# Optimization experiments

Hardware: AMD Instinct MI355X
Metric: run time of the kernel (lower is better)

The kernel has to match this reference:

```python
import jax, jax.numpy as jnp
import numpy as np

EPS = 1e-5
K_NBR = 21   # num_neighbors + 1 (self)
PSI = 4


def _bn(x, g, b):
    # BatchNorm (training-mode forward): channel-last, normalize over all other axes
    axes = tuple(range(x.ndim - 1))
    m = jnp.mean(x, axis=axes, keepdims=True)
    v = jnp.var(x, axis=axes, keepdims=True)
    return (x - m) * jax.lax.rsqrt(v + EPS) * g + b


def setup_inputs() -> dict:
    key = jax.random.key(0)
    ks = jax.random.split(key, 16)
    B, N, Cin, Cout = 4, 2048, 64, 256
    h = Cout // 2
    w_ch = Cout // PSI
    heads = 2 * PSI - 1

    def w(k, o, i):
        return jax.random.normal(k, (o, i), dtype=jnp.float32) * (1.0 / np.sqrt(i))

    p = {}
    p['xyz'] = jax.random.normal(ks[0], (B, N, 3), dtype=jnp.float32)
    p['f'] = jax.random.normal(ks[1], (B, Cin, N), dtype=jnp.float32)
    p['W_geo'] = w(ks[2], h, 6);       p['g_geo'] = jnp.ones(h);   p['b_geo'] = jnp.zeros(h)
    p['W_feat'] = w(ks[3], h, 2 * Cin); p['g_feat'] = jnp.ones(h); p['b_feat'] = jnp.zeros(h)
    p['g_bn'] = jnp.ones(Cout); p['b_bn'] = jnp.zeros(Cout)
    p['W_q'] = w(ks[4], Cout, Cout); p['g_q'] = jnp.ones(Cout); p['b_q'] = jnp.zeros(Cout)
    p['W_k'] = w(ks[5], Cout, Cout); p['g_k'] = jnp.ones(Cout); p['b_k'] = jnp.zeros(Cout)
    p['W_v'] = w(ks[6], Cout, Cout); p['g_v'] = jnp.ones(Cout); p['b_v'] = jnp.zeros(Cout)
    p['W_fus'] = w(ks[7], Cout, heads * w_ch); p['bias_fus'] = jnp.zeros(Cout)
    p['g_fus'] = jnp.ones(Cout); p['b_fus'] = jnp.zeros(Cout)
    p['g_ln'] = jnp.ones(Cout); p['b_ln'] = jnp.zeros(Cout)
    p['W_mlp'] = w(ks[8], Cout, Cout); p['bias_mlp'] = jnp.zeros(Cout)
    return p


def reference(xyz, f, W_geo, g_geo, b_geo, W_feat, g_feat, b_feat, g_bn, b_bn,
              W_q, g_q, b_q, W_k, g_k, b_k, W_v, g_v, b_v,
              W_fus, bias_fus, g_fus, b_fus, g_ln, b_ln, W_mlp, bias_mlp):
    B, N, _ = xyz.shape
    Cout = g_bn.shape[0]
    w_ch = Cout // PSI
    d_sh = w_ch // 2
    heads = 2 * PSI - 1

    # ---- PositionFusion: KNN grouping ----
    sq = jnp.sum(xyz * xyz, axis=-1)                                   # [B,N]
    d2 = sq[:, :, None] + sq[:, None, :] - 2.0 * jnp.einsum('bnd,bmd->bnm', xyz, xyz)
    _, idx = jax.lax.top_k(-d2, K_NBR)                                 # [B,N,K]

    grouped_xyz = jax.vmap(lambda p, i: p[i])(xyz, idx)                # [B,N,K,3]
    xyz_diff = grouped_xyz - xyz[:, :, None, :]
    geo_in = jnp.concatenate(
        [jnp.broadcast_to(xyz[:, :, None, :], grouped_xyz.shape), xyz_diff], axis=-1)  # [B,N,K,6]

    ft = jnp.transpose(f, (0, 2, 1))                                   # [B,N,Cin]
    grouped_f = jax.vmap(lambda p, i: p[i])(ft, idx)                   # [B,N,K,Cin]
    feat_in = jnp.concatenate(
        [grouped_f, jnp.broadcast_to(ft[:, :, None, :], grouped_f.shape)], axis=-1)    # [B,N,K,2Cin]

    geo = jax.nn.relu(_bn(jnp.einsum('bnki,oi->bnko', geo_in, W_geo), g_geo, b_geo))
    fea = jax.nn.relu(_bn(jnp.einsum('bnki,oi->bnko', feat_in, W_feat), g_feat, b_feat))
    feature_ = jnp.max(jnp.concatenate([geo, fea], axis=-1), axis=2)   # [B,N,Cout] (maxpool over K)

    # ---- BatchNorm1d ----
    x = _bn(feature_, g_bn, b_bn)

    # ---- Shifted-channel multi-head attention ----
    q = jax.nn.relu(_bn(jnp.einsum('bnc,oc->bno', x, W_q), g_q, b_q))
    k = jax.nn.relu(_bn(jnp.einsum('bnc,oc->bno', x, W_k), g_k, b_k))
    v = jax.nn.relu(_bn(jnp.einsum('bnc,oc->bno', x, W_v), g_v, b_v))

    qh = jnp.stack([q[..., m * d_sh:m * d_sh + w_ch] for m in range(heads)], axis=1)  # [B,H,N,w]
    kh = jnp.stack([k[..., m * d_sh:m * d_sh + w_ch] for m in range(heads)], axis=1)
    vh = jnp.stack([v[..., m * d_sh:m * d_sh + w_ch] for m in range(heads)], axis=1)

    a = jax.nn.softmax(jnp.einsum('bhnc,bhmc->bhnm', qh, kh), axis=-1)  # [B,H,N,N]
    o = jnp.einsum('bhnm,bhmc->bhnc', a, vh)                            # [B,H,N,w]
    O = jnp.transpose(o, (0, 2, 1, 3)).reshape(B, N, heads * w_ch)      # channel-concat per head

    fus = jax.nn.relu(_bn(jnp.einsum('bnc,oc->bno', O, W_fus) + bias_fus, g_fus, b_fus))

    feature__ = fus + feature_                                          # residual

    # ---- LayerNorm over channels ----
    m = jnp.mean(feature__, axis=-1, keepdims=True)
    var = jnp.var(feature__, axis=-1, keepdims=True)
    y = (feature__ - m) * jax.lax.rsqrt(var + EPS) * g_ln + b_ln

    out = feature__ + (jnp.einsum('bnc,oc->bno', y, W_mlp) + bias_mlp)
    return jnp.transpose(out, (0, 2, 1))                                # [B,Cout,N] like torch
```

## Files before the change

kernel.cpp:

```cpp
#include <hip/hip_runtime.h>
#include <math.h>

#define NB    4
#define NPTS  2048
#define ROWS  (NB*NPTS)
#define CIN   64
#define COUT  256
#define KNBR  21
#define NHEADS 7
#define WCH   64
#define DSH   32
#define LOG2E 1.4426950408889634f

typedef __attribute__((ext_vector_type(8))) short short8;
typedef __attribute__((ext_vector_type(4))) float floatx4;

#if __has_builtin(__builtin_amdgcn_exp2f)
#define EXP2(x) __builtin_amdgcn_exp2f(x)
#else
#define EXP2(x) __expf((x)*0.6931471805599453f)
#endif
#if __has_builtin(__builtin_amdgcn_rcpf)
#define RCP(x) __builtin_amdgcn_rcpf(x)
#else
#define RCP(x) (1.0f/(x))
#endif

__device__ __forceinline__ ushort f2bf(float x) {
    unsigned u = __float_as_uint(x);
    u += 0x7fffu + ((u >> 16) & 1u);
    return (ushort)(u >> 16);
}

__device__ __forceinline__ unsigned cvt_pk_bf16(float lo, float hi) {
    unsigned r;
    asm("v_cvt_pk_bf16_f32 %0, %1, %2" : "=v"(r) : "v"(lo), "v"(hi));
    return r;
}

template<int CTRL, int RMASK>
__device__ __forceinline__ unsigned dpp_umin_step(unsigned x) {
    unsigned t = (unsigned)__builtin_amdgcn_update_dpp((int)x, (int)x, CTRL, RMASK, 0xF, false);
    return (t < x) ? t : x;
}
__device__ __forceinline__ unsigned wave_min_u32(unsigned x) {
    x = dpp_umin_step<0x111, 0xF>(x);
    x = dpp_umin_step<0x112, 0xF>(x);
    x = dpp_umin_step<0x114, 0xF>(x);
    x = dpp_umin_step<0x118, 0xF>(x);
    x = dpp_umin_step<0x142, 0xA>(x);
    x = dpp_umin_step<0x143, 0xC>(x);
    return (unsigned)__builtin_amdgcn_readlane((int)x, 63);
}

__device__ __forceinline__ unsigned umin2(unsigned a, unsigned b) { return a < b ? a : b; }
__device__ __forceinline__ unsigned umax2(unsigned a, unsigned b) { return a < b ? b : a; }

__device__ __forceinline__ void ins6(unsigned &m1, unsigned &m2, unsigned &m3,
                                     unsigned &m4, unsigned &m5, unsigned &m6, unsigned k) {
    unsigned c = k, t;
    t = umin2(m1, c); c = umax2(m1, c); m1 = t;
    t = umin2(m2, c); c = umax2(m2, c); m2 = t;
    t = umin2(m3, c); c = umax2(m3, c); m3 = t;
    t = umin2(m4, c); c = umax2(m4, c); m4 = t;
    t = umin2(m5, c); c = umax2(m5, c); m5 = t;
    m6 = umin2(m6, c);
}

__global__ __launch_bounds__(256) void prep_knn(const float* __restrict__ f, const float* __restrict__ Wf,
                                                const float* __restrict__ xyz, const float* __restrict__ Wg,
                                                const float* __restrict__ W_q, const float* __restrict__ W_k,
                                                const float* __restrict__ W_v, const float* __restrict__ W_fus,
                                                float* __restrict__ X, float* __restrict__ A,
                                                ushort* __restrict__ Wb, float* __restrict__ sums,
                                                int* __restrict__ idx) {
    __shared__ float4 SXQ[2048];
    int t = threadIdx.x;
    int blk = blockIdx.x;
    if (blk < 512) {
        float* As = (float*)SXQ;
        float* Ws = As + 16*68;
        int bx = blk & 127, by = blk >> 7;
        if (by == 0 && bx < 12) sums[bx*256 + t] = 0.f;
        int gid = (by*128 + bx)*256 + t;
        for (int i = gid; i < 311296; i += 131072) {
            const float* Wsrc; int off;
            if (i < 65536)       { Wsrc = W_q;   off = i; }
            else if (i < 131072) { Wsrc = W_k;   off = i - 65536; }
            else if (i < 196608) { Wsrc = W_v;   off = i - 131072; }
            else                 { Wsrc = W_fus; off = i - 196608; }
            Wb[i] = f2bf(Wsrc[off]);
        }
        int r0 = bx * 64, n0 = by * 64;
        for (int e = t; e < 4096; e += 256) {
            int row = r0 + (e >> 6), c = n0 + (e & 63), cc = c & 127;
            float x = xyz[row*3], y = xyz[row*3+1], z = xyz[row*3+2];
            const float* w = Wg + cc*6;
            float s = (c < 128) ? ((w[3]*x + w[4]*y) + w[5]*z)
                                : (((w[0]-w[3])*x + (w[1]-w[4])*y) + (w[2]-w[5])*z);
            A[(size_t)row*256 + c] = s;
        }
        int b = r0 >> 11, nbase = r0 & 2047;
        int tx = t & 15, ty = t >> 4;
        float acc[4][4];
#pragma unroll
        for (int i = 0; i < 4; i++)
#pragma unroll
            for (int j = 0; j < 4; j++) acc[i][j] = 0.f;
        int m64 = t & 63, kg = t >> 6;
        int lk = t & 15, lm = t >> 4;
        for (int k0 = 0; k0 < 64; k0 += 16) {
#pragma unroll
            for (int p = 0; p < 4; p++) {
                int k = kg*4 + p;
                As[k*68 + m64] = f[(size_t)b*CIN*NPTS + (size_t)(k0 + k)*NPTS + nbase + m64];
            }
#pragma unroll
            for (int i2 = 0; i2 < 4; i2++) {
                int cg = n0 + lm + 16*i2;
                Ws[lk*68 + lm + 16*i2] = Wf[(size_t)(cg & 127)*128 + (cg >> 7)*64 + k0 + lk];
            }
            __syncthreads();
#pragma unroll
            for (int kq = 0; kq < 16; kq++) {
                float4 a  = *(const float4*)&As[kq*68 + 4*ty];
                float4 b4 = *(const float4*)&Ws[kq*68 + 4*tx];
                float av[4] = {a.x, a.y, a.z, a.w};
                float bv[4] = {b4.x, b4.y, b4.z, b4.w};
#pragma unroll
                for (int i = 0; i < 4; i++)
#pragma unroll
                    for (int j = 0; j < 4; j++) acc[i][j] = fmaf(av[i], bv[j], acc[i][j]);
            }
            __syncthreads();
        }
#pragma unroll
        for (int i = 0; i < 4; i++)
#pragma unroll
            for (int j = 0; j < 4; j++)
                X[(size_t)(r0 + 4*ty + i)*256 + n0 + 4*tx + j] = acc[i][j];
        return;
    }
    int kb = blk - 512;
    int b = kb >> 9;
    int g = kb & 511;
    for (int m = t; m < NPTS; m += 256) {
        float x = xyz[(size_t)b*NPTS*3 + m*3];
        float y = xyz[(size_t)b*NPTS*3 + m*3 + 1];
        float z = xyz[(size_t)b*NPTS*3 + m*3 + 2];
        SXQ[m] = make_float4(x, y, z, (x*x + y*y) + z*z);
    }
    __syncthreads();
    int w = t >> 6, lane = t & 63;
    int n = g*4 + w;
    float4 q4 = SXQ[n];
    float qx = q4.x, qy = q4.y, qz = q4.z, sqn = q4.w;

    unsigned key[32];
    unsigned a1 = 0xFFFFFFFFu, a2 = 0xFFFFFFFFu, a3 = 0xFFFFFFFFu,
             a4 = 0xFFFFFFFFu, a5 = 0xFFFFFFFFu, a6 = 0xFFFFFFFFu;
    unsigned c1 = 0xFFFFFFFFu, c2 = 0xFFFFFFFFu, c3 = 0xFFFFFFFFu,
             c4 = 0xFFFFFFFFu, c5 = 0xFFFFFFFFu, c6 = 0xFFFFFFFFu;
#pragma unroll
    for (int i = 0; i < 16; i++) {
        int m = lane + (i << 6);
        float4 p = SXQ[m];
        float dt = (qx*p.x + qy*p.y) + qz*p.z;
        float d2 = fmaxf((sqn + p.w) - 2.0f*dt, 0.f);
        unsigned kv = (__float_as_uint(d2) & 0xFFFFF800u) | (unsigned)m;
        key[i] = kv;
        ins6(a1, a2, a3, a4, a5, a6, kv);
    }
#pragma unroll
    for (int i = 16; i < 32; i++) {
        int m = lane + (i << 6);
        float4 p = SXQ[m];
        float dt = (qx*p.x + qy*p.y) + qz*p.z;
        float d2 = fmaxf((sqn + p.w) - 2.0f*dt, 0.f);
        unsigned kv = (__float_as_uint(d2) & 0xFFFFF800u) | (unsigned)m;
        key[i] = kv;
        ins6(c1, c2, c3, c4, c5, c6, kv);
    }
    ins6(a1, a2, a3, a4, a5, a6, c1);
    ins6(a1, a2, a3, a4, a5, a6, c2);
    ins6(a1, a2, a3, a4, a5, a6, c3);
    ins6(a1, a2, a3, a4, a5, a6, c4);
    ins6(a1, a2, a3, a4, a5, a6, c5);
    ins6(a1, a2, a3, a4, a5, a6, c6);

    unsigned winkey = 0xFFFFFFFFu;
    {
        unsigned fr = a1, p2 = a2, p3 = a3, p4 = a4, p5 = a5, p6 = a6;
#pragma unroll
        for (int kk = 0; kk < 32; kk++) {
            unsigned win = wave_min_u32(fr);
            if (lane == kk) winkey = win;
            bool own = (fr == win);
            fr = own ? p2 : fr;
            p2 = own ? p3 : p2;
            p3 = own ? p4 : p3;
            p4 = own ? p5 : p4;
            p5 = own ? p6 : p5;
            p6 = own ? 0xFFFFFFFFu : p6;
        }
        if (__ballot(fr == 0xFFFFFFFFu) != 0ULL) {
            winkey = 0xFFFFFFFFu;
            for (int kk = 0; kk < 32; kk++) {
                unsigned lv = key[0];
#pragma unroll
                for (int i = 1; i < 32; i++) lv = (key[i] < lv) ? key[i] : lv;
                unsigned win = wave_min_u32(lv);
                if (lane == kk) winkey = win;
                unsigned widx = win & 2047u;
                int slot = (int)(widx >> 6);
                bool own = (lane == (int)(widx & 63u));
#pragma unroll
                for (int i = 0; i < 32; i++)
                    if (i == slot && own) key[i] = 0xFFFFFFFFu;
            }
        }
    }
    double d2r;
    int mr;
    {
        double qx64 = (double)qx, qy64 = (double)qy, qz64 = (double)qz;
        double sqn64 = qx64*qx64 + qy64*qy64 + qz64*qz64;
        if (lane < 32) {
            mr = (int)(winkey & 2047u);
            float4 p = SXQ[mr];
            double x = (double)p.x, y = (double)p.y, z = (double)p.z;
            double sqm = x*x + y*y + z*z;
            double dt  = qx64*x + qy64*y + qz64*z;
            d2r = (sqn64 + sqm) - 2.0*dt;
        } else {
            d2r = INFINITY; mr = 0x7FFFFFFF;
        }
    }
#pragma unroll
    for (int k = 2; k <= 32; k <<= 1) {
#pragma unroll
        for (int j = k >> 1; j > 0; j >>= 1) {
            double od = __shfl_xor(d2r, j, 64);
            int    om = __shfl_xor(mr, j, 64);
            bool up    = ((lane & k) == 0);
            bool lower = ((lane & j) == 0);
            bool oless = (od < d2r) || (od == d2r && om < mr);
            bool keepOther = up ? (lower ? oless : !oless) : (lower ? !oless : oless);
            if (keepOther) { d2r = od; mr = om; }
        }
    }
    if (lane < KNBR)
        idx[((size_t)b*NPTS + n)*KNBR + lane] = mr;
}

__global__ __launch_bounds__(256) void stats_gf(const float* __restrict__ geoBC, const float* __restrict__ featAC,
                                                const int* __restrict__ idx, const float* __restrict__ g_geo,
                                                const float* __restrict__ g_feat,
                                                float* __restrict__ sums, float* __restrict__ xsel) {
    int c = threadIdx.x;
    int cc = c & 127;
    const float* base = (c < 128) ? geoBC : featAC;
    bool wantmax = ((c < 128) ? g_geo[cc] : g_feat[cc]) >= 0.f;
    float s = 0.f, ss = 0.f;
    int r0 = blockIdx.x * 32;
    for (int r = r0; r < r0 + 32; r++) {
        int b = r >> 11;
        float ctr = base[(size_t)r*256 + 128 + cc];
        float mx = -1e30f, mn = 1e30f;
        const int* ip = idx + (size_t)r*KNBR;
        for (int kk = 0; kk < KNBR; kk++) {
            int j = ip[kk];
            float xv = ctr + base[((size_t)(b*NPTS + j))*256 + cc];
            mx = fmaxf(mx, xv); mn = fminf(mn, xv);
            s += xv; ss += xv*xv;
        }
        xsel[(size_t)r*256 + c] = wantmax ? mx : mn;
    }
    atomicAdd(&sums[c], s);
    atomicAdd(&sums[256 + c], ss);
}

__global__ __launch_bounds__(256) void feature_maxsel(const float* __restrict__ xsel, const float* __restrict__ sums,
                                                      const float* __restrict__ g_geo, const float* __restrict__ b_geo,
                                                      const float* __restrict__ g_feat, const float* __restrict__ b_feat,
                                                      float* __restrict__ feat, float* __restrict__ sums_bn1) {
    int c = threadIdx.x;
    const float inv = 1.0f / (float)(ROWS*KNBR);
    float mean = sums[c]*inv;
    float var  = sums[256+c]*inv - mean*mean;
    float g  = (c < 128) ? g_geo[c] : g_feat[c-128];
    float bb = (c < 128) ? b_geo[c] : b_feat[c-128];
    float sc = g / sqrtf(var + 1e-5f);
    float tt = bb - mean*sc;
    float s = 0.f, ss = 0.f;
    int r0 = blockIdx.x*32;
    for (int r = r0; r < r0+32; r++) {
        size_t i = (size_t)r*256 + c;
        float y = fmaxf(fmaf(sc, xsel[i], tt), 0.f);
        feat[i] = y; s += y; ss += y*y;
    }
    atomicAdd(&sums_bn1[c], s); atomicAdd(&sums_bn1[256+c], ss);
}

__global__ __launch_bounds__(256) void gemm_qkv(const float* __restrict__ Af, const float* __restrict__ sums_in,
                                                const float* __restrict__ g_bn, const float* __restrict__ b_bn,
                                                const ushort* __restrict__ Wb,
                                                float* __restrict__ QKVF, float* __restrict__ sums) {
    __shared__ float bns[2][256];
    __shared__ float red[4][256][2];
    int t = threadIdx.x;
    int r0 = blockIdx.x * 64, g = blockIdx.y;
    int w = t >> 6, lane = t & 63;
    int r15 = lane & 15, quad = lane >> 4;
    {
        float mean = sums_in[512 + t] * (1.0f/(float)ROWS);
        float var  = sums_in[768 + t] * (1.0f/(float)ROWS) - mean*mean;
        float sc = g_bn[t] / sqrtf(var + 1e-5f);
        bns[0][t] = sc;
        bns[1][t] = b_bn[t] - mean*sc;
    }
    __syncthreads();
    short8 aq[8];
    {
        const float* ap = Af + (size_t)(r0 + 16*w + r15)*256;
#pragma unroll
        for (int kc = 0; kc < 8; kc++) {
            int k0 = 32*kc + 8*quad;
            float4 a0 = *(const float4*)&ap[k0];
            float4 a1 = *(const float4*)&ap[k0+4];
            float4 s0 = *(const float4*)&bns[0][k0];
            float4 s1 = *(const float4*)&bns[0][k0+4];
            float4 h0 = *(const float4*)&bns[1][k0];
            float4 h1 = *(const float4*)&bns[1][k0+4];
            ushort u8[8];
            u8[0] = f2bf(fmaf(s0.x, a0.x, h0.x)); u8[1] = f2bf(fmaf(s0.y, a0.y, h0.y));
            u8[2] = f2bf(fmaf(s0.z, a0.z, h0.z)); u8[3] = f2bf(fmaf(s0.w, a0.w, h0.w));
            u8[4] = f2bf(fmaf(s1.x, a1.x, h1.x)); u8[5] = f2bf(fmaf(s1.y, a1.y, h1.y));
            u8[6] = f2bf(fmaf(s1.z, a1.z, h1.z)); u8[7] = f2bf(fmaf(s1.w, a1.w, h1.w));
            aq[kc] = *(short8*)u8;
        }
    }
    floatx4 zero4 = {0.f, 0.f, 0.f, 0.f};
    floatx4 acc[16];
#pragma unroll
    for (int st = 0; st < 16; st++) acc[st] = zero4;
    const ushort* wbase = Wb + (size_t)g*65536 + (size_t)r15*256 + 8*quad;
#pragma unroll
    for (int st = 0; st < 16; st++) {
        const ushort* wp = wbase + (size_t)(16*st)*256;
#pragma unroll
        for (int kc = 0; kc < 8; kc++) {
            short8 bf = *(const short8*)(wp + 32*kc);
            acc[st] = __builtin_amdgcn_mfma_f32_16x16x32_bf16(aq[kc], bf, acc[st], 0, 0, 0);
        }
    }
#pragma unroll
    for (int st = 0; st < 16; st++) {
        float s  = (acc[st][0] + acc[st][1]) + (acc[st][2] + acc[st][3]);
        float q2 = (acc[st][0]*acc[st][0] + acc[st][1]*acc[st][1]) +
                   (acc[st][2]*acc[st][2] + acc[st][3]*acc[st][3]);
        s  += __shfl_xor(s, 16, 64);  s  += __shfl_xor(s, 32, 64);
        q2 += __shfl_xor(q2, 16, 64); q2 += __shfl_xor(q2, 32, 64);
        if (lane < 16) { red[w][16*st + r15][0] = s; red[w][16*st + r15][1] = q2; }
#pragma unroll
        for (int reg = 0; reg < 4; reg++)
            QKVF[(size_t)(r0 + 16*w + 4*quad + reg)*768 + g*256 + 16*st + r15] = acc[st][reg];
    }
    __syncthreads();
    {
        float s = red[0][t][0] + red[1][t][0] + red[2][t][0] + red[3][t][0];
        float q = red[0][t][1] + red[1][t][1] + red[2][t][1] + red[3][t][1];
        atomicAdd(&sums[1024 + g*512 + t], s);
        atomicAdd(&sums[1024 + g*512 + 256 + t], q);
    }
}

__global__ __launch_bounds__(256) void affine_qkv(const float* __restrict__ QKVF, const float* __restrict__ sums,
                                                  const float* __restrict__ g_q, const float* __restrict__ b_q,
                                                  const float* __restrict__ g_k, const float* __restrict__ b_k,
                                                  const float* __restrict__ g_v, const float* __restrict__ b_v,
                                                  ushort* __restrict__ qk, ushort* __restrict__ vt) {
    __shared__ float sts[6][256];
    __shared__ ushort tile[64][72];
    int t = threadIdx.x;
    {
        const float* gs[3] = {g_q, g_k, g_v};
        const float* bs[3] = {b_q, b_k, b_v};
#pragma unroll
        for (int g = 0; g < 3; g++) {
            float mean = sums[1024 + g*512 + t] * (1.0f/(float)ROWS);
            float var  = sums[1024 + g*512 + 256 + t] * (1.0f/(float)ROWS) - mean*mean;
            float sc = gs[g][t] / sqrtf(var + 1e-5f);
            float sh = bs[g][t] - mean*sc;
            if (g == 0) { sc *= LOG2E; sh *= LOG2E; }
            sts[2*g][t] = sc;
            sts[2*g+1][t] = sh;
        }
    }
    __syncthreads();
    int r0 = blockIdx.x * 64, c0 = blockIdx.y * 64;
    int b = r0 >> 11, nbase = r0 & 2047;
    if (c0 < 512) {
#pragma unroll
        for (int rep = 0; rep < 16; rep++) {
            int e = t + 256*rep;
            int row = e >> 6, c = e & 63;
            int col = c0 + c, g = col >> 8, cc = col & 255;
            float v = QKVF[(size_t)(r0 + row)*768 + col];
            v = fmaxf(fmaf(sts[2*g][cc], v, sts[2*g+1][cc]), 0.f);
            qk[(size_t)(r0 + row)*512 + col] = f2bf(v);
        }
    } else {
#pragma unroll
        for (int rep = 0; rep < 16; rep++) {
            int e = t + 256*rep;
            int row = e >> 6, c = e & 63;
            int col = c0 + c, cc = col & 255;
            float v = QKVF[(size_t)(r0 + row)*768 + col];
            v = fmaxf(fmaf(sts[4][cc], v, sts[5][cc]), 0.f);
            tile[c][row] = f2bf(v);
        }
        __syncthreads();
#pragma unroll
        for (int rep = 0; rep < 16; rep++) {
            int e = t + 256*rep;
            int cc = e >> 6, nn = e & 63;
            vt[((size_t)(b*256 + (c0 - 512) + cc))*2048 + nbase + nn] = tile[cc][nn];
        }
    }
}

__global__ __launch_bounds__(256) void attn2(const ushort* __restrict__ qk, const ushort* __restrict__ vt,
                                             float* __restrict__ obuf) {
    __shared__ ushort Ksh[2][64*72];
    __shared__ ushort Psh[128*72];
    int h = blockIdx.y, b = blockIdx.z;
    int r0 = blockIdx.x * 128;
    int t = threadIdx.x;
    int w = t >> 6, lane = t & 63;
    int r15 = lane & 15, quad = lane >> 4;
    size_t rowbase = (size_t)b*NPTS;
    int hoff = h*DSH;

    int rr0 = t >> 3, c8 = t & 7;
    const ushort* ksrc = qk + (rowbase + rr0)*512 + 256 + hoff + 8*c8;
    int ldst = rr0*72 + 8*c8;

    const ushort* vsrc = vt + ((size_t)(b*256 + hoff + r15))*2048 + 8*quad;

    short8 aq[2][2];
#pragma unroll
    for (int u = 0; u < 2; u++)
#pragma unroll
        for (int s = 0; s < 2; s++)
            aq[u][s] = *(const short8*)(qk + (rowbase + r0 + 32*w + 16*u + r15)*512 + hoff + 32*s + 8*quad);

    {
        uint4 k0 = *(const uint4*)(ksrc);
        uint4 k1 = *(const uint4*)(ksrc + 32*512);
        *(uint4*)&Ksh[0][ldst] = k0;
        *(uint4*)&Ksh[0][ldst + 32*72] = k1;
    }

    floatx4 zero4 = {0.f, 0.f, 0.f, 0.f};
    floatx4 oacc[2][4];
    float mrun[2], lrun[2];
#pragma unroll
    for (int u = 0; u < 2; u++) {
        mrun[u] = -1e30f; lrun[u] = 0.f;
#pragma unroll
        for (int i = 0; i < 4; i++) oacc[u][i] = zero4;
    }

    ushort* prow0 = &Psh[(32*w + r15)*72];
    ushort* prow1 = &Psh[(32*w + 16 + r15)*72];

    asm volatile("s_waitcnt lgkmcnt(0)" ::: "memory");
    __builtin_amdgcn_s_barrier();
    __builtin_amdgcn_sched_barrier(0);

    int cur = 0;
    for (int m0 = 0; m0 < NPTS; m0 += 64) {
        int mnext = (m0 + 64 < NPTS) ? (m0 + 64) : 0;
        uint4 kreg0 = *(const uint4*)(ksrc + (size_t)mnext*512);
        uint4 kreg1 = *(const uint4*)(ksrc + (size_t)mnext*512 + 32*512);

        short8 vreg[2][4];
#pragma unroll
        for (int s = 0; s < 2; s++)
#pragma unroll
            for (int td = 0; td < 4; td++)
                vreg[s][td] = *(const short8*)(vsrc + (size_t)(16*td)*2048 + m0 + 32*s);

        const ushort* Kc = Ksh[cur];

        floatx4 sacc[2][4];
#pragma unroll
        for (int u = 0; u < 2; u++)
#pragma unroll
            for (int tt = 0; tt < 4; tt++) sacc[u][tt] = zero4;
        __builtin_amdgcn_s_setprio(1);
#pragma unroll
        for (int tt = 0; tt < 4; tt++) {
            int key = 16*tt + r15;
#pragma unroll
            for (int s = 0; s < 2; s++) {
                short8 kf = *(const short8*)&Kc[key*72 + 32*s + 8*quad];
                sacc[0][tt] = __builtin_amdgcn_mfma_f32_16x16x32_bf16(kf, aq[0][s], sacc[0][tt], 0, 0, 0);
                sacc[1][tt] = __builtin_amdgcn_mfma_f32_16x16x32_bf16(kf, aq[1][s], sacc[1][tt], 0, 0, 0);
            }
        }
        __builtin_amdgcn_s_setprio(0);

#pragma unroll
        for (int u = 0; u < 2; u++) {
            float mx = sacc[u][0][0];
#pragma unroll
            for (int tt = 0; tt < 4; tt++)
#pragma unroll
                for (int reg = 0; reg < 4; reg++) mx = fmaxf(mx, sacc[u][tt][reg]);
            mx = fmaxf(mx, __shfl_xor(mx, 16, 64));
            mx = fmaxf(mx, __shfl_xor(mx, 32, 64));

            if (!__all(mx <= mrun[u])) {
                float mnew = fmaxf(mrun[u], mx);
                float alpha = EXP2(mrun[u] - mnew);
                lrun[u] *= alpha;
#pragma unroll
                for (int td = 0; td < 4; td++) oacc[u][td] *= alpha;
                mrun[u] = mnew;
            }

            ushort* prow = u ? prow1 : prow0;
            float rs = 0.f;
#pragma unroll
            for (int tt = 0; tt < 4; tt++) {
                float p0 = EXP2(sacc[u][tt][0] - mrun[u]);
                float p1 = EXP2(sacc[u][tt][1] - mrun[u]);
                float p2 = EXP2(sacc[u][tt][2] - mrun[u]);
                float p3 = EXP2(sacc[u][tt][3] - mrun[u]);
                rs += (p0 + p1) + (p2 + p3);
                uint2 pk2;
                pk2.x = cvt_pk_bf16(p0, p1);
                pk2.y = cvt_pk_bf16(p2, p3);
                *(uint2*)&prow[16*tt + 4*quad] = pk2;
            }
            rs += __shfl_xor(rs, 16, 64);
            rs += __shfl_xor(rs, 32, 64);
            lrun[u] += rs;
        }

        __builtin_amdgcn_s_setprio(1);
#pragma unroll
        for (int s = 0; s < 2; s++) {
            short8 pf0 = *(const short8*)&prow0[32*s + 8*quad];
            short8 pf1 = *(const short8*)&prow1[32*s + 8*quad];
#pragma unroll
            for (int td = 0; td < 4; td++) {
                short8 vf = vreg[s][td];
                oacc[0][td] = __builtin_amdgcn_mfma_f32_16x16x32_bf16(vf, pf0, oacc[0][td], 0, 0, 0);
                oacc[1][td] = __builtin_amdgcn_mfma_f32_16x16x32_bf16(vf, pf1, oacc[1][td], 0, 0, 0);
            }
        }
        __builtin_amdgcn_s_setprio(0);

        *(uint4*)&Ksh[cur ^ 1][ldst] = kreg0;
        *(uint4*)&Ksh[cur ^ 1][ldst + 32*72] = kreg1;
        cur ^= 1;

        asm volatile("s_waitcnt lgkmcnt(0)" ::: "memory");
        __builtin_amdgcn_s_barrier();
        __builtin_amdgcn_sched_barrier(0);
    }

#pragma unroll
    for (int u = 0; u < 2; u++) {
        float invl = RCP(lrun[u]);
#pragma unroll
        for (int td = 0; td < 4; td++) {
            floatx4 o = oacc[u][td] * invl;
            *(float4*)&obuf[(rowbase + r0 + 32*w + 16*u + r15)*(size_t)(NHEADS*WCH) + h*WCH + 16*td + 4*quad] =
                *(float4*)&o;
        }
    }
}

__global__ __launch_bounds__(256) void gemm_fus(const float* __restrict__ OBUF, const ushort* __restrict__ Wb,
                                                const float* __restrict__ bias, float* __restrict__ C,
                                                float* __restrict__ sums) {
    __shared__ float red[4][128][2];
    int t = threadIdx.x;
    int r0 = blockIdx.x * 64, n0 = blockIdx.y * 128;
    int w = t >> 6, lane = t & 63;
    int r15 = lane & 15, quad = lane >> 4;
    int arow = 16*w + r15;
    short8 aq[14];
    {
        const float* p0 = OBUF + (size_t)(r0 + arow)*448;
#pragma unroll
        for (int kc = 0; kc < 14; kc++) {
            int k0 = 32*kc + 8*quad;
            float4 x0 = *(const float4*)&p0[k0];
            float4 y0 = *(const float4*)&p0[k0+4];
            ushort u8[8];
            u8[0] = f2bf(x0.x); u8[1] = f2bf(x0.y);
            u8[2] = f2bf(x0.z); u8[3] = f2bf(x0.w);
            u8[4] = f2bf(y0.x); u8[5] = f2bf(y0.y);
            u8[6] = f2bf(y0.z); u8[7] = f2bf(y0.w);
            aq[kc] = *(short8*)u8;
        }
    }
    floatx4 zero4 = {0.f, 0.f, 0.f, 0.f};
    floatx4 acc[8];
#pragma unroll
    for (int st = 0; st < 8; st++) acc[st] = zero4;
    const ushort* wbase = Wb + 196608 + (size_t)(n0 + r15)*448 + 8*quad;
#pragma unroll
    for (int st = 0; st < 8; st++) {
        const ushort* wp = wbase + (size_t)(16*st)*448;
#pragma unroll
        for (int kc = 0; kc < 14; kc++) {
            short8 bf = *(const short8*)(wp + 32*kc);
            acc[st] = __builtin_amdgcn_mfma_f32_16x16x32_bf16(aq[kc], bf, acc[st], 0, 0, 0);
        }
    }
#pragma unroll
    for (int st = 0; st < 8; st++) {
        int col = n0 + 16*st + r15;
        float bi = bias[col];
        float v0 = acc[st][0] + bi, v1 = acc[st][1] + bi, v2 = acc[st][2] + bi, v3 = acc[st][3] + bi;
        float s  = (v0 + v1) + (v2 + v3);
        float q2 = (v0*v0 + v1*v1) + (v2*v2 + v3*v3);
        s  += __shfl_xor(s, 16, 64);  s  += __shfl_xor(s, 32, 64);
        q2 += __shfl_xor(q2, 16, 64); q2 += __shfl_xor(q2, 32, 64);
        if (lane < 16) { red[w][16*st + r15][0] = s; red[w][16*st + r15][1] = q2; }
        C[(size_t)(r0 + 16*w + 4*quad + 0)*256 + col] = v0;
        C[(size_t)(r0 + 16*w + 4*quad + 1)*256 + col] = v1;
        C[(size_t)(r0 + 16*w + 4*quad + 2)*256 + col] = v2;
        C[(size_t)(r0 + 16*w + 4*quad + 3)*256 + col] = v3;
    }
    __syncthreads();
    {
        int col = t >> 1, which = t & 1;
        float v = red[0][col][which] + red[1][col][which] + red[2][col][which] + red[3][col][which];
        atomicAdd(&sums[2560 + which*256 + n0 + col], v);
    }
}

__global__ __launch_bounds__(256) void gemm_mlp_ln(const float* __restrict__ FUSP, const float* __restrict__ A,
                                                   const float* __restrict__ sums,
                                                   const float* __restrict__ g_fus, const float* __restrict__ b_fus,
                                                   const float* __restrict__ g_ln, const float* __restrict__ b_ln,
                                                   const float* __restrict__ W, const float* __restrict__ bias,
                                                   float* __restrict__ outp) {
    __shared__ float Ys[256][68];
    __shared__ float FFs[64][65];
    __shared__ float Ws[16][68];
    __shared__ float tr[64][65];
    __shared__ float SC[256], SH[256], GL[256], BL[256];
    int t = threadIdx.x;
    int r0 = blockIdx.x*64, n0 = blockIdx.y*64;
    {
        float mean0 = sums[2560 + t] * (1.0f/(float)ROWS);
        float var0  = sums[2560 + 256 + t] * (1.0f/(float)ROWS) - mean0*mean0;
        float sc = g_fus[t] / sqrtf(var0 + 1e-5f);
        SC[t] = sc; SH[t] = b_fus[t] - mean0*sc;
        GL[t] = g_ln[t]; BL[t] = b_ln[t];
    }
    __syncthreads();
    int row = t >> 2, seg = t & 3;
    size_t rb = (size_t)(r0 + row)*256;
    float4 vv[16];
    float s = 0.f, ss = 0.f;
#pragma unroll
    for (int j = 0; j < 16; j++) {
        int c = seg*64 + 4*j;
        float4 fp = *(const float4*)&FUSP[rb + c];
        float4 fe = *(const float4*)&A[rb + c];
        float4 sc4 = *(const float4*)&SC[c];
        float4 sh4 = *(const float4*)&SH[c];
        float4 v;
        v.x = fmaxf(fmaf(sc4.x, fp.x, sh4.x), 0.f) + fe.x;
        v.y = fmaxf(fmaf(sc4.y, fp.y, sh4.y), 0.f) + fe.y;
        v.z = fmaxf(fmaf(sc4.z, fp.z, sh4.z), 0.f) + fe.z;
        v.w = fmaxf(fmaf(sc4.w, fp.w, sh4.w), 0.f) + fe.w;
        vv[j] = v;
        s  += (v.x + v.y) + (v.z + v.w);
        ss += (v.x*v.x + v.y*v.y) + (v.z*v.z + v.w*v.w);
        if (seg == blockIdx.y) *(float4*)&FFs[row][4*j] = v;
    }
    s  += __shfl_xor(s, 1, 64);  s  += __shfl_xor(s, 2, 64);
    ss += __shfl_xor(ss, 1, 64); ss += __shfl_xor(ss, 2, 64);
    float mean = s * (1.f/256.f);
    float var  = ss * (1.f/256.f) - mean*mean;
    float rin  = 1.f/sqrtf(var + 1e-5f);
#pragma unroll
    for (int j = 0; j < 16; j++) {
        int c = seg*64 + 4*j;
        float4 gl = *(const float4*)&GL[c];
        float4 bl = *(const float4*)&BL[c];
        float4 v = vv[j];
        Ys[c+0][row] = (v.x - mean)*rin*gl.x + bl.x;
        Ys[c+1][row] = (v.y - mean)*rin*gl.y + bl.y;
        Ys[c+2][row] = (v.z - mean)*rin*gl.z + bl.z;
        Ys[c+3][row] = (v.w - mean)*rin*gl.w + bl.w;
    }
    __syncthreads();
    int tx = t & 15, ty = t >> 4;
    int lk = t & 15, lm = t >> 4;
    float acc[4][4];
#pragma unroll
    for (int i = 0; i < 4; i++)
#pragma unroll
        for (int j = 0; j < 4; j++) acc[i][j] = 0.f;
    for (int k0 = 0; k0 < 256; k0 += 16) {
#pragma unroll
        for (int i2 = 0; i2 < 4; i2++)
            Ws[lk][lm + 16*i2] = W[(size_t)(n0 + lm + 16*i2)*256 + k0 + lk];
        __syncthreads();
#pragma unroll
        for (int kq = 0; kq < 16; kq++) {
            float4 a  = *(const float4*)&Ys[k0 + kq][4*ty];
            float4 b4 = *(const float4*)&Ws[kq][4*tx];
            float av[4] = {a.x, a.y, a.z, a.w};
            float bv[4] = {b4.x, b4.y, b4.z, b4.w};
#pragma unroll
            for (int i = 0; i < 4; i++)
#pragma unroll
                for (int j = 0; j < 4; j++) acc[i][j] = fmaf(av[i], bv[j], acc[i][j]);
        }
        __syncthreads();
    }
#pragma unroll
    for (int i = 0; i < 4; i++)
#pragma unroll
        for (int j = 0; j < 4; j++) {
            float v = acc[i][j] + bias[n0 + 4*tx + j] + FFs[4*ty + i][4*tx + j];
            tr[4*tx + j][4*ty + i] = v;
        }
    __syncthreads();
    int b = r0 >> 11, nbase = r0 & 2047;
#pragma unroll
    for (int rep = 0; rep < 16; rep++) {
        int e = t + 256*rep;
        int cl = e >> 6, nl = e & 63;
        outp[((size_t)(b*256 + n0 + cl))*2048 + nbase + nl] = tr[cl][nl];
    }
}

extern "C" void kernel_launch(void* const* d_in, const int* in_sizes, int n_in,
                              void* d_out, int out_size, void* d_ws, size_t ws_size,
                              hipStream_t stream) {
    const float* xyz    = (const float*)d_in[0];
    const float* f      = (const float*)d_in[1];
    const float* W_geo  = (const float*)d_in[2];
    const float* g_geo  = (const float*)d_in[3];
    const float* b_geo  = (const float*)d_in[4];
    const float* W_feat = (const float*)d_in[5];
    const float* g_feat = (const float*)d_in[6];
    const float* b_feat = (const float*)d_in[7];
    const float* g_bn   = (const float*)d_in[8];
    const float* b_bn   = (const float*)d_in[9];
    const float* W_q    = (const float*)d_in[10];
    const float* g_q    = (const float*)d_in[11];
    const float* b_q    = (const float*)d_in[12];
    const float* W_k    = (const float*)d_in[13];
    const float* g_k    = (const float*)d_in[14];
    const float* b_k    = (const float*)d_in[15];
    const float* W_v    = (const float*)d_in[16];
    const float* g_v    = (const float*)d_in[17];
    const float* b_v    = (const float*)d_in[18];
    const float* W_fus  = (const float*)d_in[19];
    const float* bias_fus = (const float*)d_in[20];
    const float* g_fus  = (const float*)d_in[21];
    const float* b_fus  = (const float*)d_in[22];
    const float* g_ln   = (const float*)d_in[23];
    const float* b_ln   = (const float*)d_in[24];
    const float* W_mlp  = (const float*)d_in[25];
    const float* bias_mlp = (const float*)d_in[26];

    float* ws = (float*)d_ws;
    const size_t MBF = 262144;
    float* SUMS  = ws;
    int*   IDX   = (int*)(ws + 16384);
    float* A     = ws + 1*MBF;
    float* X     = ws + 9*MBF;
    ushort* QK16 = (ushort*)(ws + 9*MBF);
    float* FUSP  = ws + 9*MBF;
    float* CSEL  = ws + 17*MBF;
    float* QKVF  = ws + 17*MBF;
    float* OBUF  = ws + 17*MBF;
    ushort* VT16 = (ushort*)(ws + 45*MBF);
    ushort* WB16 = (ushort*)(ws + 49*MBF);

    prep_knn<<<2560, 256, 0, stream>>>(f, W_feat, xyz, W_geo, W_q, W_k, W_v, W_fus,
                                       X, A, WB16, SUMS, IDX);
    stats_gf<<<256, 256, 0, stream>>>(A, X, IDX, g_geo, g_feat, SUMS, CSEL);
    feature_maxsel<<<256, 256, 0, stream>>>(CSEL, SUMS, g_geo, b_geo, g_feat, b_feat, A, SUMS + 512);
    gemm_qkv<<<dim3(128, 3), 256, 0, stream>>>(A, SUMS, g_bn, b_bn, WB16, QKVF, SUMS);
    affine_qkv<<<dim3(128, 12), 256, 0, stream>>>(QKVF, SUMS, g_q, b_q, g_k, b_k, g_v, b_v, QK16, VT16);
    attn2<<<dim3(NPTS/128, NHEADS, NB), 256, 0, stream>>>(QK16, VT16, OBUF);
    gemm_fus<<<dim3(128, 2), 256, 0, stream>>>(OBUF, WB16, bias_fus, FUSP, SUMS);
    gemm_mlp_ln<<<dim3(128, 4), 256, 0, stream>>>(FUSP, A, SUMS, g_fus, b_fus, g_ln, b_ln,
                                                  W_mlp, bias_mlp, (float*)d_out);
}
```

Baseline: 392.6 us.

## Stage V tiles in LDS and double query rows per attention block

The attention kernel now processes 256 query rows per block with 512 threads instead of 128 rows with 256 threads, halving the number of blocks per head. V tiles are cooperatively loaded into a double-buffered LDS array alongside K, rather than each wave loading its own V fragments straight from global memory. This is meant to cut redundant global K/V traffic and per-wave global load latency across the eight waves that share each tile. In exchange it uses more LDS per block, adds LDS reads for the V fragments, and reduces grid size to 224 blocks, which may underfill the GPU.

```diff
diff --git a/kernel.cpp b/kernel.cpp
--- a/kernel.cpp
+++ b/kernel.cpp
@@ -430,23 +430,23 @@
     }
 }
 
-__global__ __launch_bounds__(256) void attn2(const ushort* __restrict__ qk, const ushort* __restrict__ vt,
+__global__ __launch_bounds__(512) void attn2(const ushort* __restrict__ qk, const ushort* __restrict__ vt,
                                              float* __restrict__ obuf) {
     __shared__ ushort Ksh[2][64*72];
-    __shared__ ushort Psh[128*72];
+    __shared__ ushort Vts[2][64*72];
+    __shared__ ushort Psh[256*72];
     int h = blockIdx.y, b = blockIdx.z;
-    int r0 = blockIdx.x * 128;
+    int r0 = blockIdx.x * 256;
     int t = threadIdx.x;
     int w = t >> 6, lane = t & 63;
     int r15 = lane & 15, quad = lane >> 4;
     size_t rowbase = (size_t)b*NPTS;
     int hoff = h*DSH;
-
-    int rr0 = t >> 3, c8 = t & 7;
-    const ushort* ksrc = qk + (rowbase + rr0)*512 + 256 + hoff + 8*c8;
-    int ldst = rr0*72 + 8*c8;
-
-    const ushort* vsrc = vt + ((size_t)(b*256 + hoff + r15))*2048 + 8*quad;
+    int rr = t >> 3, c8 = t & 7;
+
+    const ushort* ksrc = qk + (rowbase + rr)*512 + 256 + hoff + 8*c8;
+    const ushort* vsrc = vt + ((size_t)(b*256 + hoff + rr))*2048 + 8*c8;
+    int ldst = rr*72 + 8*c8;
 
     short8 aq[2][2];
 #pragma unroll
@@ -457,9 +457,9 @@
 
     {
         uint4 k0 = *(const uint4*)(ksrc);
-        uint4 k1 = *(const uint4*)(ksrc + 32*512);
+        uint4 v0 = *(const uint4*)(vsrc);
         *(uint4*)&Ksh[0][ldst] = k0;
-        *(uint4*)&Ksh[0][ldst + 32*72] = k1;
+        *(uint4*)&Vts[0][ldst] = v0;
     }
 
     floatx4 zero4 = {0.f, 0.f, 0.f, 0.f};
@@ -473,7 +473,7 @@
     }
 
     ushort* prow0 = &Psh[(32*w + r15)*72];
-    ushort* prow1 = &Psh[(32*w + 16 + r15)*72];
+    ushort* prow1 = prow0 + 16*72;
 
     asm volatile("s_waitcnt lgkmcnt(0)" ::: "memory");
     __builtin_amdgcn_s_barrier();
@@ -482,17 +482,11 @@
     int cur = 0;
     for (int m0 = 0; m0 < NPTS; m0 += 64) {
         int mnext = (m0 + 64 < NPTS) ? (m0 + 64) : 0;
-        uint4 kreg0 = *(const uint4*)(ksrc + (size_t)mnext*512);
-        uint4 kreg1 = *(const uint4*)(ksrc + (size_t)mnext*512 + 32*512);
-
-        short8 vreg[2][4];
-#pragma unroll
-        for (int s = 0; s < 2; s++)
-#pragma unroll
-            for (int td = 0; td < 4; td++)
-                vreg[s][td] = *(const short8*)(vsrc + (size_t)(16*td)*2048 + m0 + 32*s);
+        uint4 kreg = *(const uint4*)(ksrc + (size_t)mnext*512);
+        uint4 vreg = *(const uint4*)(vsrc + mnext);
 
         const ushort* Kc = Ksh[cur];
+        const ushort* Vc = Vts[cur];
 
         floatx4 sacc[2][4];
 #pragma unroll
@@ -557,15 +551,15 @@
             short8 pf1 = *(const short8*)&prow1[32*s + 8*quad];
 #pragma unroll
             for (int td = 0; td < 4; td++) {
-                short8 vf = vreg[s][td];
+                short8 vf = *(const short8*)&Vc[(16*td + r15)*72 + 32*s + 8*quad];
                 oacc[0][td] = __builtin_amdgcn_mfma_f32_16x16x32_bf16(vf, pf0, oacc[0][td], 0, 0, 0);
                 oacc[1][td] = __builtin_amdgcn_mfma_f32_16x16x32_bf16(vf, pf1, oacc[1][td], 0, 0, 0);
             }
         }
         __builtin_amdgcn_s_setprio(0);
 
-        *(uint4*)&Ksh[cur ^ 1][ldst] = kreg0;
-        *(uint4*)&Ksh[cur ^ 1][ldst + 32*72] = kreg1;
+        *(uint4*)&Ksh[cur ^ 1][ldst] = kreg;
+        *(uint4*)&Vts[cur ^ 1][ldst] = vreg;
         cur ^= 1;
 
         asm volatile("s_waitcnt lgkmcnt(0)" ::: "memory");
@@ -799,7 +793,7 @@
     feature_maxsel<<<256, 256, 0, stream>>>(CSEL, SUMS, g_geo, b_geo, g_feat, b_feat, A, SUMS + 512);
     gemm_qkv<<<dim3(128, 3), 256, 0, stream>>>(A, SUMS, g_bn, b_bn, WB16, QKVF, SUMS);
     affine_qkv<<<dim3(128, 12), 256, 0, stream>>>(QKVF, SUMS, g_q, b_q, g_k, b_k, g_v, b_v, QK16, VT16);
-    attn2<<<dim3(NPTS/128, NHEADS, NB), 256, 0, stream>>>(QK16, VT16, OBUF);
+    attn2<<<dim3(NPTS/256, NHEADS, NB), 512, 0, stream>>>(QK16, VT16, OBUF);
     gemm_fus<<<dim3(128, 2), 256, 0, stream>>>(OBUF, WB16, bias_fus, FUSP, SUMS);
     gemm_mlp_ln<<<dim3(128, 4), 256, 0, stream>>>(FUSP, A, SUMS, g_fus, b_fus, g_ln, b_ln,
                                                   W_mlp, bias_mlp, (float*)d_out);
```

Result: faster. 382.1 us (-2.7%).
